# Optimization experiments

Hardware: AMD Instinct MI355X
Metric: run time of the kernel (lower is better)

## Reference

```python
import jax, jax.numpy as jnp
import numpy as np
from jax import lax

DN = ('NCHW', 'OIHW', 'NCHW')
SAME = ((1, 1), (1, 1))
VALID = ((0, 0), (0, 0))


def conv(x, w, pad):
    return lax.conv_general_dilated(x, w, (1, 1), pad, dimension_numbers=DN)


def convT(x, w, strides):
    # inverse (transposed) conv; for kernel==stride this exactly inverts the
    # non-overlapping pooling rulebook used by spconv's SparseInverseConv2d
    return lax.conv_transpose(x, w, strides, 'VALID', dimension_numbers=DN)


def maxpool(x, k):
    return lax.reduce_window(x, -jnp.inf, lax.max, (1, 1) + k, (1, 1) + k, 'VALID')


def lrelu(x):
    return jnp.where(x >= 0, x, 0.01 * x)  # F.leaky_relu default slope


def setup_inputs() -> dict:
    key = jax.random.key(0)
    ks = jax.random.split(key, 14)
    B, C, H, W = 32, 6, 500, 128
    x = jax.random.normal(ks[0], (B, C, H, W), jnp.float32)  # fully dense => all voxels active

    def p(k, shape):
        return jax.random.normal(k, shape, jnp.float32) * 0.05

    return {
        'x': x,
        'w1': p(ks[1], (8, 6, 3, 3)),      # SubMConv2d 6->8
        'w2': p(ks[2], (16, 8, 3, 3)),     # SubMConv2d 8->16
        'w3': p(ks[3], (32, 16, 3, 3)),    # SubMConv2d 16->32
        'wmu': p(ks[4], (1, 32, 1, 5)),    # SparseConv2d 32->1, kernel (1,5)
        'wlv': p(ks[5], (1, 32, 1, 5)),
        'wu0': p(ks[6], (32, 1, 1, 5)),    # SparseInverseConv2d 1->32
        'wu1': p(ks[7], (32, 32, 5, 2)),   # inverse of pool3
        'w4': p(ks[8], (16, 32, 3, 3)),
        'wu2': p(ks[9], (16, 16, 5, 2)),   # inverse of pool2
        'w5': p(ks[10], (8, 16, 3, 3)),
        'wu3': p(ks[11], (8, 8, 2, 2)),    # inverse of pool1
        'w6': p(ks[12], (6, 8, 3, 3)),
    }


def reference(x, w1, w2, w3, wmu, wlv, wu0, wu1, w4, wu2, w5, wu3, w6):
    B = x.shape[0]
    # ---- encoder ----
    h = lrelu(conv(x, w1, SAME))        # [B,8,500,128]
    h = maxpool(h, (2, 2))              # [B,8,250,64]
    h = lrelu(conv(h, w2, SAME))        # [B,16,250,64]
    h = maxpool(h, (5, 2))              # [B,16,50,32]
    h = lrelu(conv(h, w3, SAME))        # [B,32,50,32]
    h = maxpool(h, (5, 2))              # [B,32,10,16]
    mu = conv(h, wmu, VALID)            # [B,1,10,12]
    logvar = conv(h, wlv, VALID)        # [B,1,10,12]
    # ---- reparameterise ----
    eps = jax.random.normal(jax.random.key(42), mu.shape, mu.dtype)
    z = mu + eps * jnp.exp(0.5 * logvar)
    # ---- decoder ----
    d = lrelu(convT(z, wu0, (1, 1)))    # [B,32,10,16]
    d = lrelu(convT(d, wu1, (5, 2)))    # [B,32,50,32]
    d = lrelu(conv(d, w4, SAME))        # [B,16,50,32]
    d = lrelu(convT(d, wu2, (5, 2)))    # [B,16,250,64]
    d = lrelu(conv(d, w5, SAME))        # [B,8,250,64]
    d = lrelu(convT(d, wu3, (2, 2)))    # [B,8,500,128]
    d = lrelu(conv(d, w6, SAME))        # [B,6,500,128]
    return (d, mu.reshape(B, -1), logvar.reshape(B, -1), z.reshape(B, -1))
```

## Files before the change

kernel.cpp:

```cpp
#include <hip/hip_runtime.h>
#include <stdint.h>

#define DI __device__ __forceinline__

DI float lrelu(float x){ return x >= 0.0f ? x : 0.01f*x; }

DI uint32_t rotl32(uint32_t x, int d){ return (x << d) | (x >> (32 - d)); }

DI void threefry_0_42(uint32_t& x0, uint32_t& x1){
  const uint32_t ks0 = 0u, ks1 = 42u, ks2 = 0x1BD11BF0u;
  x0 += ks0; x1 += ks1;
  #define TFR(d) { x0 += x1; x1 = rotl32(x1,(d)); x1 ^= x0; }
  TFR(13) TFR(15) TFR(26) TFR(6)  x0 += ks1; x1 += ks2 + 1u;
  TFR(17) TFR(29) TFR(16) TFR(24) x0 += ks2; x1 += ks0 + 2u;
  TFR(13) TFR(15) TFR(26) TFR(6)  x0 += ks0; x1 += ks1 + 3u;
  TFR(17) TFR(29) TFR(16) TFR(24) x0 += ks1; x1 += ks2 + 4u;
  TFR(13) TFR(15) TFR(26) TFR(6)  x0 += ks2; x1 += ks0 + 5u;
  #undef TFR
}

DI float erfinv_f32(float x){
  float w = -log1pf(-x*x);
  float p;
  if (w < 5.0f){
    w = w - 2.5f;
    p = 2.81022636e-08f;
    p = fmaf(p, w, 3.43273939e-07f);
    p = fmaf(p, w, -3.5233877e-06f);
    p = fmaf(p, w, -4.39150654e-06f);
    p = fmaf(p, w, 0.00021858087f);
    p = fmaf(p, w, -0.00125372503f);
    p = fmaf(p, w, -0.00417768164f);
    p = fmaf(p, w, 0.246640727f);
    p = fmaf(p, w, 1.50140941f);
  } else {
    w = sqrtf(w) - 3.0f;
    p = -0.000200214257f;
    p = fmaf(p, w, 0.000100950558f);
    p = fmaf(p, w, 0.00134934322f);
    p = fmaf(p, w, -0.00367342844f);
    p = fmaf(p, w, 0.00573950773f);
    p = fmaf(p, w, -0.0076224613f);
    p = fmaf(p, w, 0.00943887047f);
    p = fmaf(p, w, 1.00167406f);
    p = fmaf(p, w, 2.83297682f);
  }
  return p * x;
}

#define OUT_D_OFF   0
#define OUT_MU_OFF  12288000
#define OUT_LV_OFF  (12288000 + 3840)
#define OUT_Z_OFF   (12288000 + 7680)

__global__ __launch_bounds__(256) void k_enc1(const float* __restrict__ x,
                                              const float* __restrict__ w1,
                                              float* __restrict__ p1){
  __shared__ float tile[6*10*130];
  int tid = threadIdx.x;
  int band = blockIdx.x % 63;
  int b    = blockIdx.x / 63;
  int r0 = band*8;
  for (int idx = tid; idx < 6*10*130; idx += 256){
    int lc = idx % 130;
    int rest = idx / 130;
    int lr = rest % 10;
    int ch = rest / 10;
    int gr = r0 - 1 + lr, gc = lc - 1;
    float v = 0.0f;
    if ((unsigned)gr < 500u && (unsigned)gc < 128u)
      v = x[((b*6+ch)*500+gr)*128+gc];
    tile[idx] = v;
  }
  __syncthreads();
  int pw = tid & 63, pr = tid >> 6;
  int ph = band*4 + pr;
  float acc[2][2][8];
  #pragma unroll
  for (int a=0;a<2;a++)
    #pragma unroll
    for (int d=0;d<2;d++)
      #pragma unroll
      for (int o=0;o<8;o++) acc[a][d][o] = 0.0f;
  int base = (2*pr)*130 + 2*pw;
  #pragma unroll 2
  for (int c = 0; c < 6; ++c){
    float win[4][4];
    #pragma unroll
    for (int i=0;i<4;i++)
      #pragma unroll
      for (int j=0;j<4;j++)
        win[i][j] = tile[c*1300 + base + i*130 + j];
    #pragma unroll
    for (int kh=0;kh<3;kh++)
      #pragma unroll
      for (int kw=0;kw<3;kw++){
        float wv[8];
        #pragma unroll
        for (int o=0;o<8;o++) wv[o] = w1[((o*6+c)*3+kh)*3+kw];
        #pragma unroll
        for (int dy=0;dy<2;dy++)
          #pragma unroll
          for (int dx=0;dx<2;dx++){
            float v = win[dy+kh][dx+kw];
            #pragma unroll
            for (int o=0;o<8;o++) acc[dy][dx][o] = fmaf(v, wv[o], acc[dy][dx][o]);
          }
      }
  }
  if (ph < 250){
    #pragma unroll
    for (int o=0;o<8;o++){
      float m = fmaxf(fmaxf(acc[0][0][o], acc[0][1][o]), fmaxf(acc[1][0][o], acc[1][1][o]));
      p1[((b*8+o)*250+ph)*64+pw] = lrelu(m);
    }
  }
}

__global__ __launch_bounds__(256) void k_enc2(const float* __restrict__ in,
                                              const float* __restrict__ w2,
                                              float* __restrict__ p2){
  __shared__ float tile[8*22*66];
  int tid = threadIdx.x;
  int band = blockIdx.x % 13;
  int b    = blockIdx.x / 13;
  int r0 = band*20;
  for (int idx = tid; idx < 8*22*66; idx += 256){
    int lc = idx % 66;
    int rest = idx / 66;
    int lr = rest % 22;
    int ch = rest / 22;
    int gr = r0 - 1 + lr, gc = lc - 1;
    float v = 0.0f;
    if ((unsigned)gr < 250u && (unsigned)gc < 64u)
      v = in[((b*8+ch)*250+gr)*64+gc];
    tile[idx] = v;
  }
  __syncthreads();
  int dx = tid & 1; int u = tid >> 1;
  int pw = u & 31; int pr = (u >> 5) & 3;
  int cw = 2*pw + dx;
  int ph = band*4 + pr;
  float acc[5][16];
  #pragma unroll
  for (int dy=0;dy<5;dy++)
    #pragma unroll
    for (int o=0;o<16;o++) acc[dy][o] = 0.0f;
  int base = (5*pr)*66 + cw;
  #pragma unroll 1
  for (int c = 0; c < 8; ++c){
    float win[7][3];
    #pragma unroll
    for (int i=0;i<7;i++)
      #pragma unroll
      for (int j=0;j<3;j++)
        win[i][j] = tile[c*1452 + base + i*66 + j];
    #pragma unroll
    for (int kh=0;kh<3;kh++)
      #pragma unroll
      for (int kw=0;kw<3;kw++){
        float wv[16];
        #pragma unroll
        for (int o=0;o<16;o++) wv[o] = w2[((o*8+c)*3+kh)*3+kw];
        #pragma unroll
        for (int dy=0;dy<5;dy++){
          float v = win[dy+kh][kw];
          #pragma unroll
          for (int o=0;o<16;o++) acc[dy][o] = fmaf(v, wv[o], acc[dy][o]);
        }
      }
  }
  #pragma unroll
  for (int o=0;o<16;o++){
    float m = acc[0][o];
    #pragma unroll
    for (int dy=1;dy<5;dy++) m = fmaxf(m, acc[dy][o]);
    m = fmaxf(m, __shfl_xor(m, 1));
    if (dx == 0 && ph < 50) p2[((b*16+o)*50+ph)*32+pw] = lrelu(m);
  }
}

__global__ __launch_bounds__(256) void k_conv3(const float* __restrict__ in,
                                               const float* __restrict__ w3,
                                               float* __restrict__ outp){
  __shared__ float tile[16*10*34];
  int tid = threadIdx.x;
  int bi = blockIdx.x;
  int band = bi % 7; int oh = (bi/7) & 1; int b = bi / 14;
  int r0 = band*8;
  for (int idx = tid; idx < 16*10*34; idx += 256){
    int lc = idx % 34;
    int rest = idx / 34;
    int lr = rest % 10;
    int ch = rest / 10;
    int gr = r0 - 1 + lr, gc = lc - 1;
    float v = 0.0f;
    if ((unsigned)gr < 50u && (unsigned)gc < 32u)
      v = in[((b*16+ch)*50+gr)*32+gc];
    tile[idx] = v;
  }
  __syncthreads();
  int col = tid & 31, tr = tid >> 5;
  int h = r0 + tr;
  float acc[16];
  #pragma unroll
  for (int o=0;o<16;o++) acc[o] = 0.0f;
  int base = tr*34 + col;
  #pragma unroll 2
  for (int c = 0; c < 16; ++c){
    float win[3][3];
    #pragma unroll
    for (int i=0;i<3;i++)
      #pragma unroll
      for (int j=0;j<3;j++)
        win[i][j] = tile[c*340 + base + i*34 + j];
    #pragma unroll
    for (int kh=0;kh<3;kh++)
      #pragma unroll
      for (int kw=0;kw<3;kw++){
        float v = win[kh][kw];
        #pragma unroll
        for (int o=0;o<16;o++)
          acc[o] = fmaf(v, w3[(((oh*16+o)*16+c)*3+kh)*3+kw], acc[o]);
      }
  }
  if (h < 50){
    #pragma unroll
    for (int o=0;o<16;o++)
      outp[((b*32 + oh*16 + o)*50 + h)*32 + col] = lrelu(acc[o]);
  }
}

__global__ __launch_bounds__(256) void k_pool3(const float* __restrict__ in,
                                               float* __restrict__ outp){
  int t = blockIdx.x*256 + threadIdx.x;
  int pw = t & 15; int u = t >> 4; int ph = u % 10; u /= 10; int o = u & 31; int b = u >> 5;
  float m = -INFINITY;
  #pragma unroll
  for (int dh=0;dh<5;dh++)
    #pragma unroll
    for (int dw=0;dw<2;dw++)
      m = fmaxf(m, in[((b*32+o)*50 + 5*ph+dh)*32 + 2*pw+dw]);
  outp[((b*32+o)*10+ph)*16+pw] = m;
}

__global__ __launch_bounds__(256) void k_latent(const float* __restrict__ p3,
                                                const float* __restrict__ wmu,
                                                const float* __restrict__ wlv,
                                                float* __restrict__ outp){
  int t = blockIdx.x*256 + threadIdx.x;
  int w = t % 12; int h = (t/12) % 10; int b = t/120;
  float mu = 0.0f, lv = 0.0f;
  for (int c = 0; c < 32; ++c){
    const float* row = p3 + ((b*32+c)*10+h)*16 + w;
    #pragma unroll
    for (int kw=0;kw<5;kw++){
      float v = row[kw];
      mu = fmaf(v, wmu[c*5+kw], mu);
      lv = fmaf(v, wlv[c*5+kw], lv);
    }
  }
  uint32_t x0 = 0u, x1 = (uint32_t)t;
  threefry_0_42(x0, x1);
  uint32_t bits = x0 ^ x1;
  float f = __uint_as_float((bits >> 9) | 0x3f800000u) - 1.0f;
  const float lo = -0.99999994f;
  float uu = fmaxf(lo, f * 2.0f + lo);
  float eps = 1.41421356f * erfinv_f32(uu);
  float z = mu + eps * expf(0.5f * lv);
  outp[OUT_MU_OFF + t] = mu;
  outp[OUT_LV_OFF + t] = lv;
  outp[OUT_Z_OFF  + t] = z;
}

__global__ __launch_bounds__(256) void k_dec0(const float* __restrict__ outp,
                                              const float* __restrict__ wu0,
                                              float* __restrict__ d0){
  int t = blockIdx.x*256 + threadIdx.x;
  int w = t & 15; int u = t >> 4; int h = u % 10; u /= 10; int o = u & 31; int b = u >> 5;
  const float* z = outp + OUT_Z_OFF;
  float a = 0.0f;
  #pragma unroll
  for (int kw=0;kw<5;kw++){
    int ww = w + kw - 4;
    if ((unsigned)ww < 12u) a = fmaf(z[b*120 + h*12 + ww], wu0[o*5+kw], a);
  }
  d0[((b*32+o)*10+h)*16+w] = lrelu(a);
}

__global__ __launch_bounds__(256) void k_dec1(const float* __restrict__ d0,
                                              const float* __restrict__ wu1,
                                              float* __restrict__ d1){
  int t = blockIdx.x*256 + threadIdx.x;
  int wo = t & 31; int u = t >> 5; int ho = u % 50; u /= 50; int o = u & 31; int b = u >> 5;
  int i = ho / 5, r = ho - 5*i, jj = wo >> 1, s = wo & 1;
  const float* ip = d0 + b*5120 + i*16 + jj;
  const float* wp = wu1 + (o*32*5 + (4-r))*2 + (1-s);
  float a = 0.0f;
  #pragma unroll 8
  for (int c=0;c<32;c++) a = fmaf(ip[c*160], wp[c*10], a);
  d1[((b*32+o)*50+ho)*32+wo] = lrelu(a);
}

__global__ __launch_bounds__(256) void k_c4(const float* __restrict__ in,
                                            const float* __restrict__ w4,
                                            float* __restrict__ outp){
  __shared__ float tile[32*10*34];
  int tid = threadIdx.x;
  int bi = blockIdx.x;
  int band = bi % 7; int oh = (bi/7) & 1; int b = bi / 14;
  int r0 = band*8;
  for (int idx = tid; idx < 32*10*34; idx += 256){
    int lc = idx % 34;
    int rest = idx / 34;
    int lr = rest % 10;
    int ch = rest / 10;
    int gr = r0 - 1 + lr, gc = lc - 1;
    float v = 0.0f;
    if ((unsigned)gr < 50u && (unsigned)gc < 32u)
      v = in[((b*32+ch)*50+gr)*32+gc];
    tile[idx] = v;
  }
  __syncthreads();
  int col = tid & 31, tr = tid >> 5;
  int h = r0 + tr;
  float acc[8];
  #pragma unroll
  for (int o=0;o<8;o++) acc[o] = 0.0f;
  int base = tr*34 + col;
  #pragma unroll 2
  for (int c = 0; c < 32; ++c){
    float win[3][3];
    #pragma unroll
    for (int i=0;i<3;i++)
      #pragma unroll
      for (int j=0;j<3;j++)
        win[i][j] = tile[c*340 + base + i*34 + j];
    #pragma unroll
    for (int kh=0;kh<3;kh++)
      #pragma unroll
      for (int kw=0;kw<3;kw++){
        float v = win[kh][kw];
        #pragma unroll
        for (int o=0;o<8;o++)
          acc[o] = fmaf(v, w4[(((oh*8+o)*32+c)*3+kh)*3+kw], acc[o]);
      }
  }
  if (h < 50){
    #pragma unroll
    for (int o=0;o<8;o++)
      outp[((b*16 + oh*8 + o)*50 + h)*32 + col] = lrelu(acc[o]);
  }
}

__global__ __launch_bounds__(256) void k_u2(const float* __restrict__ d2,
                                            const float* __restrict__ wu2,
                                            float* __restrict__ d3){
  int t = blockIdx.x*256 + threadIdx.x;
  int w = t & 63; int u = t >> 6; int h = u % 250; u /= 250; int o = u & 15; int b = u >> 4;
  int i = h / 5, r = h - 5*i, jj = w >> 1, s = w & 1;
  const float* ip = d2 + b*25600 + i*32 + jj;
  const float* wp = wu2 + (o*16*5 + (4-r))*2 + (1-s);
  float a = 0.0f;
  #pragma unroll 8
  for (int c=0;c<16;c++) a = fmaf(ip[c*1600], wp[c*10], a);
  d3[((b*16+o)*250+h)*64+w] = lrelu(a);
}

__global__ __launch_bounds__(256) void k_c5(const float* __restrict__ in,
                                            const float* __restrict__ w5,
                                            float* __restrict__ outp){
  __shared__ float tile[16*6*66];
  int tid = threadIdx.x;
  int band = blockIdx.x % 63;
  int b    = blockIdx.x / 63;
  int r0 = band*4;
  for (int idx = tid; idx < 16*6*66; idx += 256){
    int lc = idx % 66;
    int rest = idx / 66;
    int lr = rest % 6;
    int ch = rest / 6;
    int gr = r0 - 1 + lr, gc = lc - 1;
    float v = 0.0f;
    if ((unsigned)gr < 250u && (unsigned)gc < 64u)
      v = in[((b*16+ch)*250+gr)*64+gc];
    tile[idx] = v;
  }
  __syncthreads();
  int col = tid & 63, tr = tid >> 6;
  int h = r0 + tr;
  float acc[8];
  #pragma unroll
  for (int o=0;o<8;o++) acc[o] = 0.0f;
  int base = tr*66 + col;
  #pragma unroll 2
  for (int c = 0; c < 16; ++c){
    float win[3][3];
    #pragma unroll
    for (int i=0;i<3;i++)
      #pragma unroll
      for (int j=0;j<3;j++)
        win[i][j] = tile[c*396 + base + i*66 + j];
    #pragma unroll
    for (int kh=0;kh<3;kh++)
      #pragma unroll
      for (int kw=0;kw<3;kw++){
        float v = win[kh][kw];
        #pragma unroll
        for (int o=0;o<8;o++)
          acc[o] = fmaf(v, w5[((o*16+c)*3+kh)*3+kw], acc[o]);
      }
  }
  if (h < 250){
    #pragma unroll
    for (int o=0;o<8;o++)
      outp[((b*8+o)*250+h)*64+col] = lrelu(acc[o]);
  }
}

__global__ __launch_bounds__(256) void k_u3(const float* __restrict__ d4,
                                            const float* __restrict__ wu3,
                                            float* __restrict__ d5){
  int t = blockIdx.x*256 + threadIdx.x;
  int w = t & 127; int u = t >> 7; int h = u % 500; u /= 500; int o = u & 7; int b = u >> 3;
  int i = h >> 1, r = h & 1, jj = w >> 1, s = w & 1;
  const float* ip = d4 + b*128000 + i*64 + jj;
  const float* wp = wu3 + (o*8*2 + (1-r))*2 + (1-s);
  float a = 0.0f;
  #pragma unroll
  for (int c=0;c<8;c++) a = fmaf(ip[c*16000], wp[c*4], a);
  d5[((b*8+o)*500+h)*128+w] = lrelu(a);
}

__global__ __launch_bounds__(256) void k_c6(const float* __restrict__ in,
                                            const float* __restrict__ w6,
                                            float* __restrict__ outp){
  __shared__ float tile[8*4*130];
  int tid = threadIdx.x;
  int band = blockIdx.x % 250;
  int b    = blockIdx.x / 250;
  int r0 = band*2;
  for (int idx = tid; idx < 8*4*130; idx += 256){
    int lc = idx % 130;
    int rest = idx / 130;
    int lr = rest & 3;
    int ch = rest >> 2;
    int gr = r0 - 1 + lr, gc = lc - 1;
    float v = 0.0f;
    if ((unsigned)gr < 500u && (unsigned)gc < 128u)
      v = in[((b*8+ch)*500+gr)*128+gc];
    tile[idx] = v;
  }
  __syncthreads();
  int col = tid & 127, tr = tid >> 7;
  int h = r0 + tr;
  float acc[6];
  #pragma unroll
  for (int o=0;o<6;o++) acc[o] = 0.0f;
  int base = tr*130 + col;
  #pragma unroll 2
  for (int c = 0; c < 8; ++c){
    float win[3][3];
    #pragma unroll
    for (int i=0;i<3;i++)
      #pragma unroll
      for (int j=0;j<3;j++)
        win[i][j] = tile[c*520 + base + i*130 + j];
    #pragma unroll
    for (int kh=0;kh<3;kh++)
      #pragma unroll
      for (int kw=0;kw<3;kw++){
        float v = win[kh][kw];
        #pragma unroll
        for (int o=0;o<6;o++)
          acc[o] = fmaf(v, w6[((o*8+c)*3+kh)*3+kw], acc[o]);
      }
  }
  #pragma unroll
  for (int o=0;o<6;o++)
    outp[((b*6+o)*500+h)*128+col] = lrelu(acc[o]);
}

extern "C" void kernel_launch(void* const* d_in, const int* in_sizes, int n_in,
                              void* d_out, int out_size, void* d_ws, size_t ws_size,
                              hipStream_t stream){
  const float* x   = (const float*)d_in[0];
  const float* w1  = (const float*)d_in[1];
  const float* w2  = (const float*)d_in[2];
  const float* w3  = (const float*)d_in[3];
  const float* wmu = (const float*)d_in[4];
  const float* wlv = (const float*)d_in[5];
  const float* wu0 = (const float*)d_in[6];
  const float* wu1 = (const float*)d_in[7];
  const float* w4  = (const float*)d_in[8];
  const float* wu2 = (const float*)d_in[9];
  const float* w5  = (const float*)d_in[10];
  const float* wu3 = (const float*)d_in[11];
  const float* w6  = (const float*)d_in[12];
  float* out = (float*)d_out;
  float* A  = (float*)d_ws;
  float* Bb = A + 4096000;

  k_enc1 <<<2016, 256, 0, stream>>>(x,  w1,  A);
  k_enc2 <<< 416, 256, 0, stream>>>(A,  w2,  Bb);
  k_conv3<<< 448, 256, 0, stream>>>(Bb, w3,  A);
  k_pool3<<< 640, 256, 0, stream>>>(A,  Bb);
  k_latent<<< 15, 256, 0, stream>>>(Bb, wmu, wlv, out);
  k_dec0 <<< 640, 256, 0, stream>>>(out, wu0, A);
  k_dec1 <<<6400, 256, 0, stream>>>(A,  wu1, Bb);
  k_c4   <<< 448, 256, 0, stream>>>(Bb, w4,  A);
  k_u2   <<<32000,256, 0, stream>>>(A,  wu2, Bb);
  k_c5   <<<2016, 256, 0, stream>>>(Bb, w5,  A);
  k_u3   <<<64000,256, 0, stream>>>(A,  wu3, Bb);
  k_c6   <<<8000, 256, 0, stream>>>(Bb, w6,  out);
}
```

Baseline: 454.5 us.

## Compute multiple outputs per thread in decoder upsample and conv kernels

The transposed-conv kernels (dec1, u2, u3) now load each input column once into registers and loop over output channels inside the thread, so one thread writes 8 or 16 channels instead of one. The c5 and c6 convolutions use larger row bands and register tiling (2 columns in c5, a 2x2 block in c6), so each weight load and shared-memory window feeds several outputs. The aim is to cut redundant global and LDS reads and the number of blocks launched. The cost is more registers per thread, fewer blocks in flight, and stores that are strided across channels.

```diff
diff --git a/kernel.cpp b/kernel.cpp
--- a/kernel.cpp
+++ b/kernel.cpp
@@ -292,14 +292,21 @@
                                               const float* __restrict__ wu1,
                                               float* __restrict__ d1){
   int t = blockIdx.x*256 + threadIdx.x;
-  int wo = t & 31; int u = t >> 5; int ho = u % 50; u /= 50; int o = u & 31; int b = u >> 5;
+  int wo = t & 31; int u = t >> 5; int ho = u % 50; u /= 50; int og = u & 3; int b = u >> 2;
   int i = ho / 5, r = ho - 5*i, jj = wo >> 1, s = wo & 1;
   const float* ip = d0 + b*5120 + i*16 + jj;
-  const float* wp = wu1 + (o*32*5 + (4-r))*2 + (1-s);
-  float a = 0.0f;
-  #pragma unroll 8
-  for (int c=0;c<32;c++) a = fmaf(ip[c*160], wp[c*10], a);
-  d1[((b*32+o)*50+ho)*32+wo] = lrelu(a);
+  float in[32];
+  #pragma unroll
+  for (int c=0;c<32;c++) in[c] = ip[c*160];
+  #pragma unroll
+  for (int oo=0;oo<8;oo++){
+    int o = og*8 + oo;
+    const float* wp = wu1 + (o*32*5 + (4-r))*2 + (1-s);
+    float a = 0.0f;
+    #pragma unroll
+    for (int c=0;c<32;c++) a = fmaf(in[c], wp[c*10], a);
+    d1[((b*32+o)*50+ho)*32+wo] = lrelu(a);
+  }
 }
 
 __global__ __launch_bounds__(256) void k_c4(const float* __restrict__ in,
@@ -357,29 +364,35 @@
                                             const float* __restrict__ wu2,
                                             float* __restrict__ d3){
   int t = blockIdx.x*256 + threadIdx.x;
-  int w = t & 63; int u = t >> 6; int h = u % 250; u /= 250; int o = u & 15; int b = u >> 4;
+  int w = t & 63; int u = t >> 6; int h = u % 250; int b = u / 250;
   int i = h / 5, r = h - 5*i, jj = w >> 1, s = w & 1;
   const float* ip = d2 + b*25600 + i*32 + jj;
-  const float* wp = wu2 + (o*16*5 + (4-r))*2 + (1-s);
-  float a = 0.0f;
-  #pragma unroll 8
-  for (int c=0;c<16;c++) a = fmaf(ip[c*1600], wp[c*10], a);
-  d3[((b*16+o)*250+h)*64+w] = lrelu(a);
+  float in[16];
+  #pragma unroll
+  for (int c=0;c<16;c++) in[c] = ip[c*1600];
+  #pragma unroll
+  for (int o=0;o<16;o++){
+    const float* wp = wu2 + (o*16*5 + (4-r))*2 + (1-s);
+    float a = 0.0f;
+    #pragma unroll
+    for (int c=0;c<16;c++) a = fmaf(in[c], wp[c*10], a);
+    d3[((b*16+o)*250+h)*64+w] = lrelu(a);
+  }
 }
 
 __global__ __launch_bounds__(256) void k_c5(const float* __restrict__ in,
                                             const float* __restrict__ w5,
                                             float* __restrict__ outp){
-  __shared__ float tile[16*6*66];
+  __shared__ float tile[16*10*66];
   int tid = threadIdx.x;
-  int band = blockIdx.x % 63;
-  int b    = blockIdx.x / 63;
-  int r0 = band*4;
-  for (int idx = tid; idx < 16*6*66; idx += 256){
+  int band = blockIdx.x % 32;
+  int b    = blockIdx.x / 32;
+  int r0 = band*8;
+  for (int idx = tid; idx < 16*10*66; idx += 256){
     int lc = idx % 66;
     int rest = idx / 66;
-    int lr = rest % 6;
-    int ch = rest / 6;
+    int lr = rest % 10;
+    int ch = rest / 10;
     int gr = r0 - 1 + lr, gc = lc - 1;
     float v = 0.0f;
     if ((unsigned)gr < 250u && (unsigned)gc < 64u)
@@ -387,34 +400,43 @@
     tile[idx] = v;
   }
   __syncthreads();
-  int col = tid & 63, tr = tid >> 6;
+  int cp = tid & 31, tr = tid >> 5;
   int h = r0 + tr;
-  float acc[8];
-  #pragma unroll
-  for (int o=0;o<8;o++) acc[o] = 0.0f;
-  int base = tr*66 + col;
+  float acc[2][8];
+  #pragma unroll
+  for (int dx=0;dx<2;dx++)
+    #pragma unroll
+    for (int o=0;o<8;o++) acc[dx][o] = 0.0f;
+  int base = tr*66 + 2*cp;
   #pragma unroll 2
   for (int c = 0; c < 16; ++c){
-    float win[3][3];
+    float win[3][4];
     #pragma unroll
     for (int i=0;i<3;i++)
       #pragma unroll
-      for (int j=0;j<3;j++)
-        win[i][j] = tile[c*396 + base + i*66 + j];
+      for (int j=0;j<4;j++)
+        win[i][j] = tile[c*660 + base + i*66 + j];
     #pragma unroll
     for (int kh=0;kh<3;kh++)
       #pragma unroll
       for (int kw=0;kw<3;kw++){
-        float v = win[kh][kw];
-        #pragma unroll
-        for (int o=0;o<8;o++)
-          acc[o] = fmaf(v, w5[((o*16+c)*3+kh)*3+kw], acc[o]);
+        float wv[8];
+        #pragma unroll
+        for (int o=0;o<8;o++) wv[o] = w5[((o*16+c)*3+kh)*3+kw];
+        #pragma unroll
+        for (int dx=0;dx<2;dx++){
+          float v = win[kh][dx+kw];
+          #pragma unroll
+          for (int o=0;o<8;o++) acc[dx][o] = fmaf(v, wv[o], acc[dx][o]);
+        }
       }
   }
   if (h < 250){
     #pragma unroll
-    for (int o=0;o<8;o++)
-      outp[((b*8+o)*250+h)*64+col] = lrelu(acc[o]);
+    for (int dx=0;dx<2;dx++)
+      #pragma unroll
+      for (int o=0;o<8;o++)
+        outp[((b*8+o)*250+h)*64 + 2*cp+dx] = lrelu(acc[dx][o]);
   }
 }
 
@@ -422,29 +444,35 @@
                                             const float* __restrict__ wu3,
                                             float* __restrict__ d5){
   int t = blockIdx.x*256 + threadIdx.x;
-  int w = t & 127; int u = t >> 7; int h = u % 500; u /= 500; int o = u & 7; int b = u >> 3;
+  int w = t & 127; int u = t >> 7; int h = u % 500; int b = u / 500;
   int i = h >> 1, r = h & 1, jj = w >> 1, s = w & 1;
   const float* ip = d4 + b*128000 + i*64 + jj;
-  const float* wp = wu3 + (o*8*2 + (1-r))*2 + (1-s);
-  float a = 0.0f;
-  #pragma unroll
-  for (int c=0;c<8;c++) a = fmaf(ip[c*16000], wp[c*4], a);
-  d5[((b*8+o)*500+h)*128+w] = lrelu(a);
+  float in[8];
+  #pragma unroll
+  for (int c=0;c<8;c++) in[c] = ip[c*16000];
+  #pragma unroll
+  for (int o=0;o<8;o++){
+    const float* wp = wu3 + (o*8*2 + (1-r))*2 + (1-s);
+    float a = 0.0f;
+    #pragma unroll
+    for (int c=0;c<8;c++) a = fmaf(in[c], wp[c*4], a);
+    d5[((b*8+o)*500+h)*128+w] = lrelu(a);
+  }
 }
 
 __global__ __launch_bounds__(256) void k_c6(const float* __restrict__ in,
                                             const float* __restrict__ w6,
                                             float* __restrict__ outp){
-  __shared__ float tile[8*4*130];
+  __shared__ float tile[8*10*130];
   int tid = threadIdx.x;
-  int band = blockIdx.x % 250;
-  int b    = blockIdx.x / 250;
-  int r0 = band*2;
-  for (int idx = tid; idx < 8*4*130; idx += 256){
+  int band = blockIdx.x % 63;
+  int b    = blockIdx.x / 63;
+  int r0 = band*8;
+  for (int idx = tid; idx < 8*10*130; idx += 256){
     int lc = idx % 130;
     int rest = idx / 130;
-    int lr = rest & 3;
-    int ch = rest >> 2;
+    int lr = rest % 10;
+    int ch = rest / 10;
     int gr = r0 - 1 + lr, gc = lc - 1;
     float v = 0.0f;
     if ((unsigned)gr < 500u && (unsigned)gc < 128u)
@@ -452,33 +480,51 @@
     tile[idx] = v;
   }
   __syncthreads();
-  int col = tid & 127, tr = tid >> 7;
-  int h = r0 + tr;
-  float acc[6];
-  #pragma unroll
-  for (int o=0;o<6;o++) acc[o] = 0.0f;
-  int base = tr*130 + col;
+  int cp = tid & 63, rp = tid >> 6;
+  float acc[2][2][6];
+  #pragma unroll
+  for (int dy=0;dy<2;dy++)
+    #pragma unroll
+    for (int dx=0;dx<2;dx++)
+      #pragma unroll
+      for (int o=0;o<6;o++) acc[dy][dx][o] = 0.0f;
+  int base = (2*rp)*130 + 2*cp;
   #pragma unroll 2
   for (int c = 0; c < 8; ++c){
-    float win[3][3];
-    #pragma unroll
-    for (int i=0;i<3;i++)
-      #pragma unroll
-      for (int j=0;j<3;j++)
-        win[i][j] = tile[c*520 + base + i*130 + j];
+    float win[4][4];
+    #pragma unroll
+    for (int i=0;i<4;i++)
+      #pragma unroll
+      for (int j=0;j<4;j++)
+        win[i][j] = tile[c*1300 + base + i*130 + j];
     #pragma unroll
     for (int kh=0;kh<3;kh++)
       #pragma unroll
       for (int kw=0;kw<3;kw++){
-        float v = win[kh][kw];
+        float wv[6];
+        #pragma unroll
+        for (int o=0;o<6;o++) wv[o] = w6[((o*8+c)*3+kh)*3+kw];
+        #pragma unroll
+        for (int dy=0;dy<2;dy++)
+          #pragma unroll
+          for (int dx=0;dx<2;dx++){
+            float v = win[dy+kh][dx+kw];
+            #pragma unroll
+            for (int o=0;o<6;o++) acc[dy][dx][o] = fmaf(v, wv[o], acc[dy][dx][o]);
+          }
+      }
+  }
+  #pragma unroll
+  for (int dy=0;dy<2;dy++){
+    int h = r0 + 2*rp + dy;
+    if (h < 500){
+      #pragma unroll
+      for (int dx=0;dx<2;dx++)
         #pragma unroll
         for (int o=0;o<6;o++)
-          acc[o] = fmaf(v, w6[((o*8+c)*3+kh)*3+kw], acc[o]);
-      }
-  }
-  #pragma unroll
-  for (int o=0;o<6;o++)
-    outp[((b*6+o)*500+h)*128+col] = lrelu(acc[o]);
+          outp[((b*6+o)*500+h)*128 + 2*cp+dx] = lrelu(acc[dy][dx][o]);
+    }
+  }
 }
 
 extern "C" void kernel_launch(void* const* d_in, const int* in_sizes, int n_in,
@@ -507,10 +553,10 @@
   k_pool3<<< 640, 256, 0, stream>>>(A,  Bb);
   k_latent<<< 15, 256, 0, stream>>>(Bb, wmu, wlv, out);
   k_dec0 <<< 640, 256, 0, stream>>>(out, wu0, A);
-  k_dec1 <<<6400, 256, 0, stream>>>(A,  wu1, Bb);
+  k_dec1 <<< 800, 256, 0, stream>>>(A,  wu1, Bb);
   k_c4   <<< 448, 256, 0, stream>>>(Bb, w4,  A);
-  k_u2   <<<32000,256, 0, stream>>>(A,  wu2, Bb);
-  k_c5   <<<2016, 256, 0, stream>>>(Bb, w5,  A);
-  k_u3   <<<64000,256, 0, stream>>>(A,  wu3, Bb);
-  k_c6   <<<8000, 256, 0, stream>>>(Bb, w6,  out);
-}
+  k_u2   <<<2000, 256, 0, stream>>>(A,  wu2, Bb);
+  k_c5   <<<1024, 256, 0, stream>>>(Bb, w5,  A);
+  k_u3   <<<8000, 256, 0, stream>>>(A,  wu3, Bb);
+  k_c6   <<<2016, 256, 0, stream>>>(Bb, w6,  out);
+}
```

Measured after the change: 432.2 us. 4.9% less time.
